# Kernel tuning notes

Hardware: AMD Instinct MI355X
Metric: run time of the kernel (lower is better)

Reference implementation:

```python
import jax, jax.numpy as jnp
import numpy as np

B = 131072
FEATURES = 64
NUM_BINS = 10
HIDDEN = 512
TAIL_BOUND = 1.0
MIN_BIN_WIDTH = 1e-3
MIN_BIN_HEIGHT = 1e-3
MIN_DERIVATIVE = 1e-3

# alternating mask [1,0,1,0,...]: mask>0 -> transform features, mask<=0 -> identity features
TRANSFORM_IDX = np.arange(0, FEATURES, 2)
IDENTITY_IDX = np.arange(1, FEATURES, 2)
D_ID = len(IDENTITY_IDX)   # 32
D_TR = len(TRANSFORM_IDX)  # 32
PARAM_PER_FEAT = 3 * NUM_BINS - 1  # tails='linear' -> 29
PARAM_DIM = D_TR * PARAM_PER_FEAT  # 928


def setup_inputs() -> dict:
    key = jax.random.key(0)
    k = jax.random.split(key, 3)
    x = jax.random.normal(k[0], (B, FEATURES), jnp.float32)
    W1 = jax.random.normal(k[1], (D_ID, HIDDEN), jnp.float32) / np.sqrt(D_ID)
    b1 = jnp.zeros((HIDDEN,), jnp.float32)
    W2 = jax.random.normal(k[2], (HIDDEN, PARAM_DIM), jnp.float32) / np.sqrt(HIDDEN)
    b2 = jnp.zeros((PARAM_DIM,), jnp.float32)
    return {"x": x, "W1": W1, "b1": b1, "W2": W2, "b2": b2}


def _rqs(x, uw, uh, ud):
    """Unconstrained rational-quadratic spline with linear tails, forward direction.
    x: [B, D]; uw, uh: [B, D, NUM_BINS]; ud: [B, D, NUM_BINS-1].
    Returns (outputs [B,D], logabsdet [B,D])."""
    inside = (x >= -TAIL_BOUND) & (x <= TAIL_BOUND)
    xc = jnp.clip(x, -TAIL_BOUND, TAIL_BOUND)
    # pad derivatives so boundary derivatives equal 1 (softplus(const)+md == 1)
    const = np.log(np.exp(1.0 - MIN_DERIVATIVE) - 1.0)
    ud = jnp.pad(ud, [(0, 0), (0, 0), (1, 1)], constant_values=const)
    nb = NUM_BINS

    widths = jax.nn.softmax(uw, axis=-1)
    widths = MIN_BIN_WIDTH + (1 - MIN_BIN_WIDTH * nb) * widths
    cumw = jnp.pad(jnp.cumsum(widths, axis=-1), [(0, 0), (0, 0), (1, 0)])
    cumw = 2 * TAIL_BOUND * cumw - TAIL_BOUND
    cumw = cumw.at[..., 0].set(-TAIL_BOUND).at[..., -1].set(TAIL_BOUND)
    widths = cumw[..., 1:] - cumw[..., :-1]

    derivs = MIN_DERIVATIVE + jax.nn.softplus(ud)  # [B, D, nb+1]

    heights = jax.nn.softmax(uh, axis=-1)
    heights = MIN_BIN_HEIGHT + (1 - MIN_BIN_HEIGHT * nb) * heights
    cumh = jnp.pad(jnp.cumsum(heights, axis=-1), [(0, 0), (0, 0), (1, 0)])
    cumh = 2 * TAIL_BOUND * cumh - TAIL_BOUND
    cumh = cumh.at[..., 0].set(-TAIL_BOUND).at[..., -1].set(TAIL_BOUND)
    heights = cumh[..., 1:] - cumh[..., :-1]

    # bin search (nflows-style searchsorted with eps on last edge)
    locs = cumw.at[..., -1].add(1e-6)
    idx = jnp.sum((xc[..., None] >= locs).astype(jnp.int32), axis=-1) - 1
    idx = jnp.clip(idx, 0, nb - 1)[..., None]

    g = lambda t: jnp.take_along_axis(t, idx, axis=-1)[..., 0]
    in_cw = g(cumw)
    in_w = g(widths)
    in_ch = g(cumh)
    in_h = g(heights)
    in_delta = g(heights / widths)
    d_k = g(derivs)
    d_k1 = jnp.take_along_axis(derivs, idx + 1, axis=-1)[..., 0]

    theta = (xc - in_cw) / in_w
    t1m = theta * (1 - theta)
    numer = in_h * (in_delta * theta ** 2 + d_k * t1m)
    denom = in_delta + (d_k + d_k1 - 2 * in_delta) * t1m
    y = in_ch + numer / denom
    dnum = in_delta ** 2 * (d_k1 * theta ** 2 + 2 * in_delta * t1m + d_k * (1 - theta) ** 2)
    lad = jnp.log(dnum) - 2 * jnp.log(denom)
    # linear tails: identity outside [-B, B], logabsdet 0
    return jnp.where(inside, y, x), jnp.where(inside, lad, 0.0)


def reference(x, W1, b1, W2, b2):
    ident = x[:, IDENTITY_IDX]   # [B, D_ID]
    trans = x[:, TRANSFORM_IDX]  # [B, D_TR]
    # transform_net: 1-hidden-layer MLP
    h = jax.nn.relu(ident @ W1 + b1)
    params = (h @ W2 + b2).reshape(x.shape[0], D_TR, PARAM_PER_FEAT)
    scale = 1.0 / np.sqrt(HIDDEN)  # hidden_features scaling branch
    uw = params[..., :NUM_BINS] * scale
    uh = params[..., NUM_BINS:2 * NUM_BINS] * scale
    ud = params[..., 2 * NUM_BINS:]
    y_tr, lad = _rqs(trans, uw, uh, ud)
    logabsdet = jnp.sum(lad, axis=1)  # sum_except_batch
    out = jnp.zeros_like(x).at[:, IDENTITY_IDX].set(ident).at[:, TRANSFORM_IDX].set(y_tr)
    ot_cost = jnp.sum((x - out) ** 2, axis=-1)
    return out, logabsdet, ot_cost
```

## Files before the change

kernel.cpp:

```cpp
#include <hip/hip_runtime.h>
#include <math.h>

#define NROWS 131072
#define BM 64
#define NBLK (NROWS / BM)
#define NB 10
#define PPF 29
#define NRAW 928
#define NPAD 1024
#define HID 512
#define THREADS 1024

typedef _Float16 half8 __attribute__((ext_vector_type(8)));
typedef float f32x4 __attribute__((ext_vector_type(4)));

#define W1T_OFF (1 << 20)

#define HSTR 1040
#define LDS_B 66560
#define SMEM_BYTES (66560 + 65536)
#define PSTR 937

__device__ __forceinline__ void async_copy16(const void* g, void* l) {
    __builtin_amdgcn_global_load_lds(
        (const __attribute__((address_space(1))) unsigned int*)g,
        (__attribute__((address_space(3))) unsigned int*)l, 16, 0, 0);
}

__global__ __launch_bounds__(256) void prep_w2(const float* __restrict__ W2,
                                               _Float16* __restrict__ W2S) {
    int flat = blockIdx.x * 256 + threadIdx.x;
    int n  = flat & 1023;
    int kg = flat >> 10;
    int ks = kg >> 2, g = kg & 3;
    half8 o;
    #pragma unroll
    for (int j = 0; j < 8; ++j) {
        int k = ks * 32 + g * 8 + j;
        float v = (n < NRAW) ? W2[(size_t)k * NRAW + n] : 0.f;
        o[j] = (_Float16)v;
    }
    size_t addr = (size_t)ks * 65536 + (size_t)n * 64 + ((g ^ ((n >> 1) & 3)) << 4);
    *(half8*)((char*)W2S + addr) = o;
}

__global__ __launch_bounds__(256) void prep_w1(const float* __restrict__ W1,
                                               _Float16* __restrict__ W1T) {
    int idx = blockIdx.x * 256 + threadIdx.x;
    int n = idx >> 5, k = idx & 31;
    W1T[n * 32 + k] = (_Float16)W1[k * HID + n];
}

__device__ __forceinline__ float softplusf(float v) {
    return fmaxf(v, 0.f) + log1pf(expf(-fabsf(v)));
}

__global__ __launch_bounds__(THREADS, 4) void flow_main(
    const float* __restrict__ x,
    const float* __restrict__ b1,
    const float* __restrict__ b2,
    const _Float16* __restrict__ W2S,
    const _Float16* __restrict__ W1T,
    float* __restrict__ out,
    float* __restrict__ lad_out,
    float* __restrict__ ot_out)
{
    __shared__ __align__(16) char smem[SMEM_BYTES];
    __shared__ float sb2[NRAW];
    const int tid = threadIdx.x;
    const int w   = tid >> 6;
    const int l   = tid & 63;
    const int l15 = l & 15;
    const int g   = l >> 4;
    const int wr  = w >> 3;
    const int wc  = w & 7;
    const int row0 = blockIdx.x * BM;

    {
        const char* gsrc0 = (const char*)W2S + (size_t)(w * 4096) + (size_t)l * 16;
        char* ldst = smem + LDS_B + w * 4096;
        #pragma unroll
        for (int i = 0; i < 4; ++i)
            async_copy16(gsrc0 + i * 1024, ldst + i * 1024);
    }

    {
        const float4* xv = (const float4*)(x + (size_t)row0 * 64);
        float4* ov = (float4*)(out + (size_t)row0 * 64);
        ov[tid] = xv[tid];
    }
    if (tid < NRAW) sb2[tid] = b2[tid];

    {
        half8 a1[4];
        #pragma unroll
        for (int mt1 = 0; mt1 < 4; ++mt1) {
            const float4* xr = (const float4*)(x + (size_t)(row0 + mt1 * 16 + l15) * 64 + g * 16);
            float4 q0 = xr[0], q1 = xr[1], q2 = xr[2], q3 = xr[3];
            half8 a;
            a[0] = (_Float16)q0.y; a[1] = (_Float16)q0.w;
            a[2] = (_Float16)q1.y; a[3] = (_Float16)q1.w;
            a[4] = (_Float16)q2.y; a[5] = (_Float16)q2.w;
            a[6] = (_Float16)q3.y; a[7] = (_Float16)q3.w;
            a1[mt1] = a;
        }
        #pragma unroll
        for (int nt = 0; nt < 2; ++nt) {
            int n1 = w * 32 + nt * 16 + l15;
            half8 bf = *(const half8*)((const char*)W1T + (size_t)n1 * 64 + g * 16);
            float bias = b1[n1];
            #pragma unroll
            for (int mt1 = 0; mt1 < 4; ++mt1) {
                f32x4 c = {0.f, 0.f, 0.f, 0.f};
                c = __builtin_amdgcn_mfma_f32_16x16x32_f16(a1[mt1], bf, c, 0, 0, 0);
                #pragma unroll
                for (int r = 0; r < 4; ++r) {
                    float hv = fmaxf(c[r] + bias, 0.f);
                    *(_Float16*)(smem + (mt1 * 16 + g * 4 + r) * HSTR + n1 * 2) = (_Float16)hv;
                }
            }
        }
    }
    __syncthreads();

    f32x4 acc[2][8];
    #pragma unroll
    for (int mt = 0; mt < 2; ++mt)
        #pragma unroll
        for (int j = 0; j < 8; ++j) acc[mt][j] = (f32x4){0.f, 0.f, 0.f, 0.f};

    const int hbase = (wr * 32 + l15) * HSTR + g * 16;
    const int n0 = wc * 128 + l15;
    const int bbase = LDS_B + n0 * 64 + ((g ^ ((n0 >> 1) & 3)) << 4);
    const char* gsrc = (const char*)W2S + 65536 + (size_t)(w * 4096) + (size_t)l * 16;
    char* ldst = smem + LDS_B + w * 4096;

    for (int ks = 0; ks < 16; ++ks) {
        half8 a0 = *(const half8*)(smem + hbase + ks * 64);
        half8 a1 = *(const half8*)(smem + hbase + 16640 + ks * 64);
        half8 bf[8];
        #pragma unroll
        for (int j = 0; j < 8; ++j)
            if (wc < 7 || j < 2) bf[j] = *(const half8*)(smem + bbase + j * 1024);
        __syncthreads();
        if (ks < 15) {
            #pragma unroll
            for (int i = 0; i < 4; ++i)
                async_copy16(gsrc + i * 1024, ldst + i * 1024);
            gsrc += 65536;
        }
        #pragma unroll
        for (int j = 0; j < 8; ++j) {
            if (wc < 7 || j < 2) {
                acc[0][j] = __builtin_amdgcn_mfma_f32_16x16x32_f16(a0, bf[j], acc[0][j], 0, 0, 0);
                acc[1][j] = __builtin_amdgcn_mfma_f32_16x16x32_f16(a1, bf[j], acc[1][j], 0, 0, 0);
            }
        }
        __syncthreads();
    }

    const float SCALE = 0.04419417382415922f;
    #pragma unroll
    for (int pass = 0; pass < 2; ++pass) {
        __syncthreads();
        if (wr == pass) {
            #pragma unroll
            for (int mt = 0; mt < 2; ++mt)
                #pragma unroll
                for (int j = 0; j < 8; ++j) {
                    int n = wc * 128 + j * 16 + l15;
                    if (n < NRAW) {
                        #pragma unroll
                        for (int r = 0; r < 4; ++r)
                            *(float*)(smem + ((mt * 16 + g * 4 + r) * PSTR + n) * 4) = acc[mt][j][r];
                    }
                }
        }
        __syncthreads();

        const int row_l = tid >> 5;
        const int f = tid & 31;
        const int grow = row0 + pass * 32 + row_l;
        const char* pb = smem + ((size_t)row_l * PSTR + (size_t)f * PPF) * 4;
        const float* bp = sb2 + f * PPF;

        float uw[NB];
        #pragma unroll
        for (int j = 0; j < NB; ++j)
            uw[j] = (*(const float*)(pb + j * 4) + bp[j]) * SCALE;
        float mw = uw[0];
        #pragma unroll
        for (int j = 1; j < NB; ++j) mw = fmaxf(mw, uw[j]);
        float sw = 0.f;
        #pragma unroll
        for (int j = 0; j < NB; ++j) { uw[j] = expf(uw[j] - mw); sw += uw[j]; }
        float invw = 1.f / sw;
        float cw[NB + 1];
        cw[0] = -1.f;
        float cum = 0.f;
        #pragma unroll
        for (int j = 0; j < NB; ++j) {
            cum += 0.001f + 0.99f * uw[j] * invw;
            cw[j + 1] = 2.f * cum - 1.f;
        }
        cw[NB] = 1.f;

        #pragma unroll
        for (int j = 0; j < NB; ++j)
            uw[j] = (*(const float*)(pb + (NB + j) * 4) + bp[NB + j]) * SCALE;
        float mh = uw[0];
        #pragma unroll
        for (int j = 1; j < NB; ++j) mh = fmaxf(mh, uw[j]);
        float sh = 0.f;
        #pragma unroll
        for (int j = 0; j < NB; ++j) { uw[j] = expf(uw[j] - mh); sh += uw[j]; }
        float invh = 1.f / sh;
        float ch[NB + 1];
        ch[0] = -1.f;
        float cumh = 0.f;
        #pragma unroll
        for (int j = 0; j < NB; ++j) {
            cumh += 0.001f + 0.99f * uw[j] * invh;
            ch[j + 1] = 2.f * cumh - 1.f;
        }
        ch[NB] = 1.f;

        float dv[NB + 1];
        dv[0] = 1.0f;
        dv[NB] = 1.0f;
        #pragma unroll
        for (int j = 0; j < NB - 1; ++j)
            dv[j + 1] = 0.001f + softplusf(*(const float*)(pb + (2 * NB + j) * 4) + bp[2 * NB + j]);

        const float xv = x[(size_t)grow * 64 + 2 * f];
        float xc = fminf(fmaxf(xv, -1.f), 1.f);
        int idx = 0;
        #pragma unroll
        for (int j = 1; j <= NB - 1; ++j) idx += (xc >= cw[j]) ? 1 : 0;
        float in_cw = cw[0], cwn = cw[1];
        float in_ch = ch[0], chn = ch[1];
        float dk = dv[0], dk1 = dv[1];
        #pragma unroll
        for (int j = 1; j <= NB - 1; ++j) {
            bool cnd = (idx >= j);
            in_cw = cnd ? cw[j] : in_cw;
            cwn   = cnd ? cw[j + 1] : cwn;
            in_ch = cnd ? ch[j] : in_ch;
            chn   = cnd ? ch[j + 1] : chn;
            dk    = cnd ? dv[j] : dk;
            dk1   = cnd ? dv[j + 1] : dk1;
        }
        float in_w  = cwn - in_cw;
        float in_h  = chn - in_ch;
        float delta = in_h / in_w;
        float th    = (xc - in_cw) / in_w;
        float t1m   = th * (1.f - th);
        float th2   = th * th;
        float numer = in_h * (delta * th2 + dk * t1m);
        float denom = delta + (dk + dk1 - 2.f * delta) * t1m;
        float y     = in_ch + numer / denom;
        float omt   = 1.f - th;
        float dnum  = delta * delta * (dk1 * th2 + 2.f * delta * t1m + dk * omt * omt);
        float lad   = logf(dnum) - 2.f * logf(denom);

        bool inside = (xv >= -1.f) && (xv <= 1.f);
        float yo = inside ? y : xv;
        out[(size_t)grow * 64 + 2 * f] = yo;
        float ladp = inside ? lad : 0.f;
        float dd = xv - yo;
        float otp = dd * dd;

        #pragma unroll
        for (int m = 1; m < 32; m <<= 1) {
            ladp += __shfl_xor(ladp, m);
            otp  += __shfl_xor(otp, m);
        }
        if ((tid & 31) == 0) {
            lad_out[grow] = ladp;
            ot_out[grow]  = otp;
        }
    }
}

extern "C" void kernel_launch(void* const* d_in, const int* in_sizes, int n_in,
                              void* d_out, int out_size, void* d_ws, size_t ws_size,
                              hipStream_t stream) {
    const float* x  = (const float*)d_in[0];
    const float* W1 = (const float*)d_in[1];
    const float* b1 = (const float*)d_in[2];
    const float* W2 = (const float*)d_in[3];
    const float* b2 = (const float*)d_in[4];
    float* out = (float*)d_out;
    float* lad = out + (size_t)NROWS * 64;
    float* otc = lad + NROWS;

    char* wsb = (char*)d_ws;
    _Float16* W2S = (_Float16*)wsb;
    _Float16* W1T = (_Float16*)(wsb + W1T_OFF);

    hipLaunchKernelGGL(prep_w2, dim3(256), dim3(256), 0, stream, W2, W2S);
    hipLaunchKernelGGL(prep_w1, dim3(64), dim3(256), 0, stream, W1, W1T);
    hipLaunchKernelGGL(flow_main, dim3(NBLK), dim3(THREADS), 0, stream,
                       x, b1, b2, W2S, W1T, out, lad, otc);
}
```

Baseline: 529.4 us.

## Split N dimension across blocks, fuse layer-1 recompute into K loop, add partial reduction

Each block now handles 128 rows by a 256-column slice of the padded 1024-wide parameter matrix (4 N-blocks), with W2 repacked per feature into 32-column groups. The hidden activations are no longer stored whole in LDS; each K-step recomputes its 32-wide hidden slice with MFMA from W1 and stages it through a small per-wave scratch. This cuts LDS use and allows more blocks per CU. The cost is that layer 1 is recomputed once per N-block, and per-row logabsdet and transport-cost partials go through global memory into a separate reduce kernel. A separate copy kernel now writes the identity features to the output.

```diff
diff --git a/kernel.cpp b/kernel.cpp
--- a/kernel.cpp
+++ b/kernel.cpp
@@ -1,25 +1,32 @@
 #include <hip/hip_runtime.h>
 #include <math.h>
 
-#define NROWS 131072
-#define BM 64
-#define NBLK (NROWS / BM)
+#define M 131072
+#define BM 128
 #define NB 10
 #define PPF 29
-#define NRAW 928
-#define NPAD 1024
 #define HID 512
-#define THREADS 1024
+#define N2 1024
+#define BN 256
+#define NBN 4
+#define THREADS 512
+#define NKS 16
 
 typedef _Float16 half8 __attribute__((ext_vector_type(8)));
 typedef float f32x4 __attribute__((ext_vector_type(4)));
 
+#define W2P_OFF 0
 #define W1T_OFF (1 << 20)
-
-#define HSTR 1040
-#define LDS_B 66560
-#define SMEM_BYTES (66560 + 65536)
-#define PSTR 937
+#define LADP_OFF (2 << 20)
+#define OTP_OFF  (4 << 20)
+
+#define STG  0
+#define WSCR 16384
+#define OVR  0
+#define SB1  68608
+#define SB2  70656
+#define SMEM_BYTES 71584
+#define PSTR 268
 
 __device__ __forceinline__ void async_copy16(const void* g, void* l) {
     __builtin_amdgcn_global_load_lds(
@@ -27,21 +34,29 @@
         (__attribute__((address_space(3))) unsigned int*)l, 16, 0, 0);
 }
 
+__device__ __forceinline__ unsigned pkh(float a, float b) {
+    union { _Float16 h[2]; unsigned u; } v;
+    v.h[0] = (_Float16)a; v.h[1] = (_Float16)b;
+    return v.u;
+}
+
 __global__ __launch_bounds__(256) void prep_w2(const float* __restrict__ W2,
-                                               _Float16* __restrict__ W2S) {
+                                               _Float16* __restrict__ W2P) {
     int flat = blockIdx.x * 256 + threadIdx.x;
-    int n  = flat & 1023;
+    int col = flat & 1023;
     int kg = flat >> 10;
     int ks = kg >> 2, g = kg & 3;
+    int f = col >> 5, p = col & 31;
     half8 o;
     #pragma unroll
     for (int j = 0; j < 8; ++j) {
         int k = ks * 32 + g * 8 + j;
-        float v = (n < NRAW) ? W2[(size_t)k * NRAW + n] : 0.f;
+        float v = (p < PPF) ? W2[(size_t)k * 928 + f * PPF + p] : 0.f;
         o[j] = (_Float16)v;
     }
-    size_t addr = (size_t)ks * 65536 + (size_t)n * 64 + ((g ^ ((n >> 1) & 3)) << 4);
-    *(half8*)((char*)W2S + addr) = o;
+    size_t addr = (size_t)ks * 65536 + (size_t)(col >> 8) * 16384
+                + (size_t)(col & 255) * 64 + ((g ^ ((col >> 1) & 3)) << 4);
+    *(half8*)((char*)W2P + addr) = o;
 }
 
 __global__ __launch_bounds__(256) void prep_w1(const float* __restrict__ W1,
@@ -51,6 +66,15 @@
     W1T[n * 32 + k] = (_Float16)W1[k * HID + n];
 }
 
+__global__ __launch_bounds__(256) void copy_x(const float* __restrict__ x,
+                                              float* __restrict__ out) {
+    const float4* xv = (const float4*)x;
+    float4* ov = (float4*)out;
+    int base = blockIdx.x * 1024 + threadIdx.x;
+    #pragma unroll
+    for (int q = 0; q < 4; ++q) ov[base + q * 256] = xv[base + q * 256];
+}
+
 __device__ __forceinline__ float softplusf(float v) {
     return fmaxf(v, 0.f) + log1pf(expf(-fabsf(v)));
 }
@@ -59,67 +83,47 @@
     const float* __restrict__ x,
     const float* __restrict__ b1,
     const float* __restrict__ b2,
-    const _Float16* __restrict__ W2S,
+    const _Float16* __restrict__ W2P,
     const _Float16* __restrict__ W1T,
     float* __restrict__ out,
-    float* __restrict__ lad_out,
-    float* __restrict__ ot_out)
+    float* __restrict__ ladp,
+    float* __restrict__ otp)
 {
     __shared__ __align__(16) char smem[SMEM_BYTES];
-    __shared__ float sb2[NRAW];
     const int tid = threadIdx.x;
     const int w   = tid >> 6;
     const int l   = tid & 63;
     const int l15 = l & 15;
     const int g   = l >> 4;
-    const int wr  = w >> 3;
-    const int wc  = w & 7;
-    const int row0 = blockIdx.x * BM;
-
+    const int wm  = w >> 1;
+    const int nh  = w & 1;
+    const int bid = (blockIdx.x & 7) * 512 + (blockIdx.x >> 3);
+    const int mblk = bid >> 2, nblk = bid & 3;
+    const int row0 = mblk * BM;
+
+    const int lsw = (l15 >> 1) & 3;
+
+    const char* gW = (const char*)W2P + (size_t)nblk * 16384 + w * 2048 + (size_t)l * 16;
     {
-        const char* gsrc0 = (const char*)W2S + (size_t)(w * 4096) + (size_t)l * 16;
-        char* ldst = smem + LDS_B + w * 4096;
-        #pragma unroll
-        for (int i = 0; i < 4; ++i)
-            async_copy16(gsrc0 + i * 1024, ldst + i * 1024);
-    }
-
-    {
-        const float4* xv = (const float4*)(x + (size_t)row0 * 64);
-        float4* ov = (float4*)(out + (size_t)row0 * 64);
-        ov[tid] = xv[tid];
-    }
-    if (tid < NRAW) sb2[tid] = b2[tid];
-
-    {
-        half8 a1[4];
-        #pragma unroll
-        for (int mt1 = 0; mt1 < 4; ++mt1) {
-            const float4* xr = (const float4*)(x + (size_t)(row0 + mt1 * 16 + l15) * 64 + g * 16);
-            float4 q0 = xr[0], q1 = xr[1], q2 = xr[2], q3 = xr[3];
-            half8 a;
-            a[0] = (_Float16)q0.y; a[1] = (_Float16)q0.w;
-            a[2] = (_Float16)q1.y; a[3] = (_Float16)q1.w;
-            a[4] = (_Float16)q2.y; a[5] = (_Float16)q2.w;
-            a[6] = (_Float16)q3.y; a[7] = (_Float16)q3.w;
-            a1[mt1] = a;
-        }
-        #pragma unroll
-        for (int nt = 0; nt < 2; ++nt) {
-            int n1 = w * 32 + nt * 16 + l15;
-            half8 bf = *(const half8*)((const char*)W1T + (size_t)n1 * 64 + g * 16);
-            float bias = b1[n1];
-            #pragma unroll
-            for (int mt1 = 0; mt1 < 4; ++mt1) {
-                f32x4 c = {0.f, 0.f, 0.f, 0.f};
-                c = __builtin_amdgcn_mfma_f32_16x16x32_f16(a1[mt1], bf, c, 0, 0, 0);
-                #pragma unroll
-                for (int r = 0; r < 4; ++r) {
-                    float hv = fmaxf(c[r] + bias, 0.f);
-                    *(_Float16*)(smem + (mt1 * 16 + g * 4 + r) * HSTR + n1 * 2) = (_Float16)hv;
-                }
-            }
-        }
+        char* dst = smem + STG + w * 2048;
+        async_copy16(gW, dst);
+        async_copy16(gW + 1024, dst + 1024);
+    }
+
+    ((float*)(smem + SB1))[tid] = b1[tid];
+    if (tid < 232) ((float*)(smem + SB2))[tid] = b2[nblk * 232 + tid];
+
+    half8 xf[2];
+    #pragma unroll
+    for (int mt = 0; mt < 2; ++mt) {
+        const float4* xr = (const float4*)(x + (size_t)(row0 + wm * 32 + mt * 16 + l15) * 64 + g * 16);
+        float4 q0 = xr[0], q1 = xr[1], q2 = xr[2], q3 = xr[3];
+        half8 a;
+        a[0] = (_Float16)q0.y; a[1] = (_Float16)q0.w;
+        a[2] = (_Float16)q1.y; a[3] = (_Float16)q1.w;
+        a[4] = (_Float16)q2.y; a[5] = (_Float16)q2.w;
+        a[6] = (_Float16)q3.y; a[7] = (_Float16)q3.w;
+        xf[mt] = a;
     }
     __syncthreads();
 
@@ -129,32 +133,46 @@
         #pragma unroll
         for (int j = 0; j < 8; ++j) acc[mt][j] = (f32x4){0.f, 0.f, 0.f, 0.f};
 
-    const int hbase = (wr * 32 + l15) * HSTR + g * 16;
-    const int n0 = wc * 128 + l15;
-    const int bbase = LDS_B + n0 * 64 + ((g ^ ((n0 >> 1) & 3)) << 4);
-    const char* gsrc = (const char*)W2S + 65536 + (size_t)(w * 4096) + (size_t)l * 16;
-    char* ldst = smem + LDS_B + w * 4096;
-
-    for (int ks = 0; ks < 16; ++ks) {
-        half8 a0 = *(const half8*)(smem + hbase + ks * 64);
-        half8 a1 = *(const half8*)(smem + hbase + 16640 + ks * 64);
+    char* wscr = smem + WSCR + w * 2048;
+    const int bfoff = STG + (nh * 128 + l15) * 64 + ((g ^ lsw) << 4);
+
+    for (int ks = 0; ks < NKS; ++ks) {
+        half8 w1f0 = *(const half8*)((const char*)W1T + (size_t)(ks * 32 + l15) * 64 + g * 16);
+        half8 w1f1 = *(const half8*)((const char*)W1T + (size_t)(ks * 32 + 16 + l15) * 64 + g * 16);
+        float4 bv0 = *(const float4*)(smem + SB1 + (ks * 32 + g * 4) * 4);
+        float4 bv1 = *(const float4*)(smem + SB1 + (ks * 32 + 16 + g * 4) * 4);
+        half8 af[2];
+        #pragma unroll
+        for (int mt = 0; mt < 2; ++mt) {
+            f32x4 d0 = {0.f, 0.f, 0.f, 0.f}, d1 = {0.f, 0.f, 0.f, 0.f};
+            d0 = __builtin_amdgcn_mfma_f32_16x16x32_f16(w1f0, xf[mt], d0, 0, 0, 0);
+            d1 = __builtin_amdgcn_mfma_f32_16x16x32_f16(w1f1, xf[mt], d1, 0, 0, 0);
+            unsigned p00 = pkh(fmaxf(d0[0] + bv0.x, 0.f), fmaxf(d0[1] + bv0.y, 0.f));
+            unsigned p01 = pkh(fmaxf(d0[2] + bv0.z, 0.f), fmaxf(d0[3] + bv0.w, 0.f));
+            unsigned p10 = pkh(fmaxf(d1[0] + bv1.x, 0.f), fmaxf(d1[1] + bv1.y, 0.f));
+            unsigned p11 = pkh(fmaxf(d1[2] + bv1.z, 0.f), fmaxf(d1[3] + bv1.w, 0.f));
+            char* wb = wscr + mt * 1024 + l15 * 64 + (g & 1) * 8;
+            *(uint2*)(wb + ((((g >> 1)) ^ lsw) << 4))     = make_uint2(p00, p01);
+            *(uint2*)(wb + (((2 + (g >> 1)) ^ lsw) << 4)) = make_uint2(p10, p11);
+            af[mt] = *(const half8*)(wscr + mt * 1024 + l15 * 64 + ((g ^ lsw) << 4));
+        }
+
         half8 bf[8];
         #pragma unroll
-        for (int j = 0; j < 8; ++j)
-            if (wc < 7 || j < 2) bf[j] = *(const half8*)(smem + bbase + j * 1024);
+        for (int nf = 0; nf < 8; ++nf)
+            bf[nf] = *(const half8*)(smem + bfoff + nf * 1024);
         __syncthreads();
-        if (ks < 15) {
-            #pragma unroll
-            for (int i = 0; i < 4; ++i)
-                async_copy16(gsrc + i * 1024, ldst + i * 1024);
-            gsrc += 65536;
-        }
-        #pragma unroll
-        for (int j = 0; j < 8; ++j) {
-            if (wc < 7 || j < 2) {
-                acc[0][j] = __builtin_amdgcn_mfma_f32_16x16x32_f16(a0, bf[j], acc[0][j], 0, 0, 0);
-                acc[1][j] = __builtin_amdgcn_mfma_f32_16x16x32_f16(a1, bf[j], acc[1][j], 0, 0, 0);
-            }
+
+        if (ks < NKS - 1) {
+            const char* src = gW + (size_t)(ks + 1) * 65536;
+            char* dst = smem + STG + w * 2048;
+            async_copy16(src, dst);
+            async_copy16(src + 1024, dst + 1024);
+        }
+        #pragma unroll
+        for (int nf = 0; nf < 8; ++nf) {
+            acc[0][nf] = __builtin_amdgcn_mfma_f32_16x16x32_f16(af[0], bf[nf], acc[0][nf], 0, 0, 0);
+            acc[1][nf] = __builtin_amdgcn_mfma_f32_16x16x32_f16(af[1], bf[nf], acc[1][nf], 0, 0, 0);
         }
         __syncthreads();
     }
@@ -162,27 +180,27 @@
     const float SCALE = 0.04419417382415922f;
     #pragma unroll
     for (int pass = 0; pass < 2; ++pass) {
-        __syncthreads();
-        if (wr == pass) {
+        if (pass == 1) __syncthreads();
+        if ((wm >> 1) == pass) {
             #pragma unroll
             for (int mt = 0; mt < 2; ++mt)
                 #pragma unroll
-                for (int j = 0; j < 8; ++j) {
-                    int n = wc * 128 + j * 16 + l15;
-                    if (n < NRAW) {
-                        #pragma unroll
-                        for (int r = 0; r < 4; ++r)
-                            *(float*)(smem + ((mt * 16 + g * 4 + r) * PSTR + n) * 4) = acc[mt][j][r];
-                    }
+                for (int nf = 0; nf < 8; ++nf) {
+                    int col = nh * 128 + nf * 16 + l15;
+                    int cb = (col >> 5) * 33 + (col & 31);
+                    int rb = (wm & 1) * 32 + mt * 16 + g * 4;
+                    #pragma unroll
+                    for (int r = 0; r < 4; ++r)
+                        *(float*)(smem + OVR + ((rb + r) * PSTR + cb) * 4) = acc[mt][nf][r];
                 }
         }
         __syncthreads();
 
-        const int row_l = tid >> 5;
-        const int f = tid & 31;
-        const int grow = row0 + pass * 32 + row_l;
-        const char* pb = smem + ((size_t)row_l * PSTR + (size_t)f * PPF) * 4;
-        const float* bp = sb2 + f * PPF;
+        const int row_l = tid >> 3;
+        const int f_l = tid & 7;
+        const int grow = row0 + pass * 64 + row_l;
+        const char* pb = smem + OVR + ((size_t)row_l * PSTR + (size_t)f_l * 33) * 4;
+        const float* bp = (const float*)(smem + SB2) + f_l * PPF;
 
         float uw[NB];
         #pragma unroll
@@ -232,7 +250,8 @@
         for (int j = 0; j < NB - 1; ++j)
             dv[j + 1] = 0.001f + softplusf(*(const float*)(pb + (2 * NB + j) * 4) + bp[2 * NB + j]);
 
-        const float xv = x[(size_t)grow * 64 + 2 * f];
+        const int f_glob = nblk * 8 + f_l;
+        const float xv = x[(size_t)grow * 64 + 2 * f_glob];
         float xc = fminf(fmaxf(xv, -1.f), 1.f);
         int idx = 0;
         #pragma unroll
@@ -265,21 +284,36 @@
 
         bool inside = (xv >= -1.f) && (xv <= 1.f);
         float yo = inside ? y : xv;
-        out[(size_t)grow * 64 + 2 * f] = yo;
-        float ladp = inside ? lad : 0.f;
+        out[(size_t)grow * 64 + 2 * f_glob] = yo;
+        float ladv = inside ? lad : 0.f;
         float dd = xv - yo;
-        float otp = dd * dd;
-
-        #pragma unroll
-        for (int m = 1; m < 32; m <<= 1) {
-            ladp += __shfl_xor(ladp, m);
-            otp  += __shfl_xor(otp, m);
-        }
-        if ((tid & 31) == 0) {
-            lad_out[grow] = ladp;
-            ot_out[grow]  = otp;
-        }
-    }
+        float otv = dd * dd;
+
+        #pragma unroll
+        for (int m = 1; m < 8; m <<= 1) {
+            ladv += __shfl_xor(ladv, m);
+            otv  += __shfl_xor(otv, m);
+        }
+        if (f_l == 0) {
+            ladp[(size_t)nblk * M + grow] = ladv;
+            otp[(size_t)nblk * M + grow]  = otv;
+        }
+    }
+}
+
+__global__ __launch_bounds__(256) void reduce_k(const float* __restrict__ ladp,
+                                                const float* __restrict__ otp,
+                                                float* __restrict__ lad_out,
+                                                float* __restrict__ ot_out) {
+    int r = blockIdx.x * 256 + threadIdx.x;
+    float s = 0.f, t = 0.f;
+    #pragma unroll
+    for (int nb = 0; nb < NBN; ++nb) {
+        s += ladp[(size_t)nb * M + r];
+        t += otp[(size_t)nb * M + r];
+    }
+    lad_out[r] = s;
+    ot_out[r]  = t;
 }
 
 extern "C" void kernel_launch(void* const* d_in, const int* in_sizes, int n_in,
@@ -291,15 +325,20 @@
     const float* W2 = (const float*)d_in[3];
     const float* b2 = (const float*)d_in[4];
     float* out = (float*)d_out;
-    float* lad = out + (size_t)NROWS * 64;
-    float* otc = lad + NROWS;
+    float* lad = out + (size_t)M * 64;
+    float* otc = lad + M;
 
     char* wsb = (char*)d_ws;
-    _Float16* W2S = (_Float16*)wsb;
+    _Float16* W2P = (_Float16*)(wsb + W2P_OFF);
     _Float16* W1T = (_Float16*)(wsb + W1T_OFF);
-
-    hipLaunchKernelGGL(prep_w2, dim3(256), dim3(256), 0, stream, W2, W2S);
+    float* ladp = (float*)(wsb + LADP_OFF);
+    float* otp  = (float*)(wsb + OTP_OFF);
+
+    hipLaunchKernelGGL(prep_w2, dim3(256), dim3(256), 0, stream, W2, W2P);
     hipLaunchKernelGGL(prep_w1, dim3(64), dim3(256), 0, stream, W1, W1T);
-    hipLaunchKernelGGL(flow_main, dim3(NBLK), dim3(THREADS), 0, stream,
-                       x, b1, b2, W2S, W1T, out, lad, otc);
-}
+    hipLaunchKernelGGL(copy_x, dim3(2048), dim3(256), 0, stream, x, out);
+    hipLaunchKernelGGL(flow_main, dim3(4096), dim3(THREADS), 0, stream,
+                       x, b1, b2, W2P, W1T, out, ladp, otp);
+    hipLaunchKernelGGL(reduce_k, dim3(512), dim3(256), 0, stream,
+                       ladp, otp, lad, otc);
+}
```

Result: faster. 478.0 us (-9.7%).
